# Optimization experiments

Hardware: AMD Instinct MI355X
Metric: run time of the kernel (lower is better)

The kernel has to match this reference:

```python
import jax, jax.numpy as jnp
import numpy as np

KERNEL = 8


def setup_inputs() -> dict:
    key = jax.random.key(0)
    ks = jax.random.split(key, 9)
    N, Cin, L = 16, 128, 2048
    Cout = 256
    x = jax.random.normal(ks[0], (N, Cin, L), dtype=jnp.float32)
    conv_w = jax.random.normal(ks[1], (Cout, Cin, KERNEL), dtype=jnp.float32) * (1.0 / np.sqrt(Cin * KERNEL))
    conv_b = jax.random.normal(ks[2], (Cout,), dtype=jnp.float32) * 0.01
    wq = jax.random.normal(ks[3], (Cout, Cout), dtype=jnp.float32) * (1.0 / np.sqrt(Cout))
    bq = jax.random.normal(ks[4], (Cout,), dtype=jnp.float32) * 0.01
    wk = jax.random.normal(ks[5], (Cout, Cout), dtype=jnp.float32) * (1.0 / np.sqrt(Cout))
    bk = jax.random.normal(ks[6], (Cout,), dtype=jnp.float32) * 0.01
    wv = jax.random.normal(ks[7], (Cout, Cout), dtype=jnp.float32) * (1.0 / np.sqrt(Cout))
    bv = jax.random.normal(ks[8], (Cout,), dtype=jnp.float32) * 0.01
    return {"x": x, "conv_w": conv_w, "conv_b": conv_b,
            "wq": wq, "bq": bq, "wk": wk, "bk": bk, "wv": wv, "bv": bv}


def reference(x, conv_w, conv_b, wq, bq, wk, bk, wv, bv):
    # Conv1d, valid padding: [N, Cin, L] -> [N, Cout, S], S = L - KERNEL + 1
    h = jax.lax.conv_general_dilated(
        x, conv_w, window_strides=(1,), padding='VALID',
        dimension_numbers=('NCH', 'OIH', 'NCH'))
    h = jax.nn.relu(h + conv_b[None, :, None])
    N, C, S = h.shape
    h = jnp.transpose(h, (0, 2, 1))  # [N, S, C]
    # Linear layers (torch convention: y = x @ W^T + b)
    q = jnp.einsum('nsc,dc->nsd', h, wq) + bq
    k = jnp.einsum('nsc,dc->nsd', h, wk) + bk
    v = jnp.einsum('nsc,dc->nsd', h, wv) + bv
    # sigmoid (non-normalized) attention over full SxS scores
    scores = jnp.einsum('nsd,ntd->nst', q, k) / jnp.sqrt(jnp.asarray(C, h.dtype))
    attn = jax.nn.sigmoid(scores)  # [N, S, S]
    out = jnp.einsum('nst,ntd->nsd', attn, v)
    return jnp.transpose(out, (0, 2, 1))  # [N, C, S]
```

## Files before the change

kernel.cpp:

```cpp
#include <hip/hip_runtime.h>

typedef short short8 __attribute__((ext_vector_type(8)));
typedef float f32x4 __attribute__((ext_vector_type(4)));
typedef float f32x16 __attribute__((ext_vector_type(16)));
typedef unsigned short u16x4 __attribute__((ext_vector_type(4)));

constexpr int NB = 16, CIN = 128, LIN = 2048, CO = 256;
constexpr int SL = 2041;
constexpr int MP = 32768;
constexpr int XTS = 136;


constexpr size_t XT_OFF = 0;
constexpr size_t XT_SZ  = (size_t)NB*LIN*XTS*2 + 65536;
constexpr size_t CW_OFF = XT_OFF + XT_SZ;
constexpr size_t CW_SZ  = (size_t)CO*CIN*8*2;
constexpr size_t WQ_OFF = CW_OFF + CW_SZ;
constexpr size_t WB_SZ  = (size_t)CO*CO*2;
constexpr size_t WK_OFF = WQ_OFF + WB_SZ;
constexpr size_t WV_OFF = WK_OFF + WB_SZ;
constexpr size_t H_OFF  = WV_OFF + WB_SZ;
constexpr size_t HB_SZ  = (size_t)MP*CO*2;
constexpr size_t Q_OFF  = H_OFF + HB_SZ;
constexpr size_t K_OFF  = Q_OFF + HB_SZ;
constexpr size_t VT_OFF = K_OFF + HB_SZ;

__device__ inline unsigned short f2bf(float f) {
  union { float f; unsigned int u; } v; v.f = f;
  unsigned int r = v.u + 0x7fffu + ((v.u >> 16) & 1u);
  return (unsigned short)(r >> 16);
}

__device__ inline void sync_lds() {
  __asm__ volatile("" ::: "memory");
  __builtin_amdgcn_s_waitcnt(0xc07f);
  __builtin_amdgcn_s_barrier();
  __asm__ volatile("" ::: "memory");
}
__device__ inline void barrier_only() {
  __asm__ volatile("" ::: "memory");
  __builtin_amdgcn_s_barrier();
  __asm__ volatile("" ::: "memory");
}

#if defined(__has_builtin)
#if __has_builtin(__builtin_amdgcn_global_load_lds)
#define HAVE_GLDS 1
#endif
#endif

__device__ inline void gld16(const unsigned short* g, void* l) {
#ifdef HAVE_GLDS
  __builtin_amdgcn_global_load_lds(
      (const __attribute__((address_space(1))) void*)g,
      (__attribute__((address_space(3))) void*)l, 16, 0, 0);
#else
  *(short8*)l = *(const short8*)g;
#endif
}

__global__ __launch_bounds__(256) void prep_kernel(
    const float* __restrict__ x, unsigned short* __restrict__ xt,
    const float* __restrict__ cw_in, unsigned short* __restrict__ cw_out,
    const float* __restrict__ wq, const float* __restrict__ wk, const float* __restrict__ wv,
    unsigned short* __restrict__ wqb, unsigned short* __restrict__ wkb,
    unsigned short* __restrict__ wvb) {
  __shared__ float tile[32][33];
  const int b = blockIdx.x;
  const int tid = threadIdx.x;
  if (b < 4096) {
    const int tx = tid & 31, ty = tid >> 5;
    const int s0 = (b & 63) * 32, c0 = ((b >> 6) & 3) * 32, n = b >> 8;
    #pragma unroll
    for (int r = 0; r < 4; ++r)
      tile[ty * 4 + r][tx] = x[((size_t)(n * CIN + c0 + ty * 4 + r)) * LIN + s0 + tx];
    __syncthreads();
    #pragma unroll
    for (int r = 0; r < 4; ++r)
      xt[((size_t)(n * LIN + s0 + ty * 4 + r)) * XTS + c0 + tx] = f2bf(tile[tx][ty * 4 + r]);
  } else if (b < 4096 + 1024) {
    int idx = (b - 4096) * 256 + tid;
    int co = idx >> 10, r = idx & 1023, kp = r >> 7, ci = r & 127;
    cw_out[idx] = f2bf(cw_in[co * 1024 + ci * 8 + kp]);
  } else {
    int lb2 = b - (4096 + 1024);
    int z = lb2 >> 6, lb = lb2 & 63;
    const float* src = (z == 0) ? wq : (z == 1) ? wk : wv;
    unsigned short* dst = (z == 0) ? wqb : (z == 1) ? wkb : wvb;
    int i = (lb * 256 + tid) * 4;
    float4 v = *(const float4*)(src + i);
    u16x4 r;
    r.x = f2bf(v.x); r.y = f2bf(v.y); r.z = f2bf(v.z); r.w = f2bf(v.w);
    *(u16x4*)(dst + i) = r;
  }
}

__global__ __launch_bounds__(256) void conv_gemm(
    const unsigned short* __restrict__ xt,
    const unsigned short* __restrict__ wb,
    const float* __restrict__ bias,
    unsigned short* __restrict__ h)
{
  __shared__ unsigned short sX[18432];
  __shared__ unsigned short sB[2][4096];
  const int tid = threadIdx.x;
  const int w = tid >> 6, lane = tid & 63, quad = lane >> 4, l16 = lane & 15;
  const int n  = blockIdx.y;
  const int s0 = blockIdx.x * 128;
  const int d0 = blockIdx.z * 128;

  {
    const unsigned short* xbase = xt + ((size_t)n * LIN + s0) * XTS;
    #pragma unroll
    for (int i = 0; i < 9; ++i) {
      int u = i * 256 + tid;
      gld16(xbase + u * 8, ((char*)sX) + u * 16);
    }
  }

  const int brow0 = tid >> 2, bkgs = tid & 3;
  short8 breg[2];
  #pragma unroll
  for (int i2 = 0; i2 < 2; ++i2) {
    int row = i2 * 64 + brow0;
    int kg = bkgs ^ ((row >> 1) & 3);
    breg[i2] = *(const short8*)(wb + (size_t)(d0 + row) * 1024 + kg * 8);
  }
  #pragma unroll
  for (int i2 = 0; i2 < 2; ++i2)
    *(short8*)(&sB[0][(i2 * 256 + tid) * 8]) = breg[i2];
  __syncthreads();

  f32x4 acc[2][8];
  #pragma unroll
  for (int i = 0; i < 2; ++i)
    #pragma unroll
    for (int j = 0; j < 8; ++j) acc[i][j] = (f32x4){0.f, 0.f, 0.f, 0.f};

  for (int kc = 0; kc < 32; ++kc) {
    const int kcn = (kc < 31) ? kc + 1 : kc;
    const int kpn = kcn >> 2, ci0n = (kcn & 3) * 32;
    #pragma unroll
    for (int i2 = 0; i2 < 2; ++i2) {
      int row = i2 * 64 + brow0;
      int kg = bkgs ^ ((row >> 1) & 3);
      breg[i2] = *(const short8*)(wb + (size_t)(d0 + row) * 1024 + kpn * 128 + ci0n + kg * 8);
    }

    const int kp = kc >> 2, ci0 = (kc & 3) * 32;
    const unsigned short* sBc = sB[kc & 1];
    short8 bfr[8];
    #pragma unroll
    for (int j = 0; j < 8; ++j) {
      int r = j * 16 + l16;
      bfr[j] = *(const short8*)(sBc + r * 32 + (quad ^ ((r >> 1) & 3)) * 8);
    }
    #pragma unroll
    for (int i = 0; i < 2; ++i) {
      int srow = w * 32 + i * 16 + l16;
      short8 afr = *(const short8*)(sX + (srow + kp) * XTS + ci0 + quad * 8);
      #pragma unroll
      for (int j = 0; j < 8; ++j)
        acc[i][j] = __builtin_amdgcn_mfma_f32_16x16x32_bf16(afr, bfr[j], acc[i][j], 0, 0, 0);
    }

    #pragma unroll
    for (int i2 = 0; i2 < 2; ++i2)
      *(short8*)(&sB[(kc + 1) & 1][(i2 * 256 + tid) * 8]) = breg[i2];
    sync_lds();
  }

  #pragma unroll
  for (int i = 0; i < 2; ++i)
    #pragma unroll
    for (int j = 0; j < 8; ++j) {
      int col = d0 + j * 16 + l16;
      float bv = bias[col];
      #pragma unroll
      for (int jj = 0; jj < 4; ++jj) {
        int s = s0 + w * 32 + i * 16 + quad * 4 + jj;
        if (s < SL) {
          float val = fmaxf(acc[i][j][jj] + bv, 0.f);
          h[(size_t)(n * 2048 + s) * CO + col] = f2bf(val);
        }
      }
    }
}

__global__ __launch_bounds__(256) void lin_gemm(
    const unsigned short* __restrict__ A,
    const unsigned short* __restrict__ Bq, const unsigned short* __restrict__ Bk,
    const unsigned short* __restrict__ Bv,
    const float* __restrict__ biq, const float* __restrict__ bik,
    const float* __restrict__ biv,
    unsigned short* __restrict__ qb, unsigned short* __restrict__ kb,
    unsigned short* __restrict__ vtb)
{
  __shared__ unsigned short smem[16384];
  unsigned short* const sAb = smem;
  unsigned short* const sBb = smem + 8192;
  const int tid = threadIdx.x;
  const int w = tid >> 6, lane = tid & 63, quad = lane >> 4, l16 = lane & 15;
  const int m0 = blockIdx.x * 128, d0 = blockIdx.y * 128, z = blockIdx.z;
  const unsigned short* B = (z == 0) ? Bq : (z == 1) ? Bk : Bv;
  const float* bias        = (z == 0) ? biq : (z == 1) ? bik : biv;

  const int brow0 = tid >> 2, bkgs = tid & 3;
  short8 areg[2], breg[2];
  #pragma unroll
  for (int i2 = 0; i2 < 2; ++i2) {
    int row = i2 * 64 + brow0;
    int kg = bkgs ^ ((row >> 1) & 3);
    areg[i2] = *(const short8*)(A + (size_t)(m0 + row) * CO + kg * 8);
    breg[i2] = *(const short8*)(B + (size_t)(d0 + row) * CO + kg * 8);
  }
  #pragma unroll
  for (int i2 = 0; i2 < 2; ++i2) {
    *(short8*)(sAb + (i2 * 256 + tid) * 8) = areg[i2];
    *(short8*)(sBb + (i2 * 256 + tid) * 8) = breg[i2];
  }
  sync_lds();

  f32x4 acc[2][8];
  #pragma unroll
  for (int i = 0; i < 2; ++i)
    #pragma unroll
    for (int j = 0; j < 8; ++j) acc[i][j] = (f32x4){0.f, 0.f, 0.f, 0.f};

  for (int kc = 0; kc < 8; ++kc) {
    const int kcn = (kc < 7) ? kc + 1 : kc;
    #pragma unroll
    for (int i2 = 0; i2 < 2; ++i2) {
      int row = i2 * 64 + brow0;
      int kg = bkgs ^ ((row >> 1) & 3);
      areg[i2] = *(const short8*)(A + (size_t)(m0 + row) * CO + kcn * 32 + kg * 8);
      breg[i2] = *(const short8*)(B + (size_t)(d0 + row) * CO + kcn * 32 + kg * 8);
    }

    const unsigned short* sAc = sAb + (kc & 1) * 4096;
    const unsigned short* sBc = sBb + (kc & 1) * 4096;
    short8 afr[2], bfr[8];
    #pragma unroll
    for (int i = 0; i < 2; ++i) {
      int r = w * 32 + i * 16 + l16;
      afr[i] = *(const short8*)(sAc + r * 32 + (quad ^ ((r >> 1) & 3)) * 8);
    }
    #pragma unroll
    for (int j = 0; j < 8; ++j) {
      int r = j * 16 + l16;
      bfr[j] = *(const short8*)(sBc + r * 32 + (quad ^ ((r >> 1) & 3)) * 8);
    }
    #pragma unroll
    for (int i = 0; i < 2; ++i)
      #pragma unroll
      for (int j = 0; j < 8; ++j)
        acc[i][j] = __builtin_amdgcn_mfma_f32_16x16x32_bf16(afr[i], bfr[j], acc[i][j], 0, 0, 0);

    #pragma unroll
    for (int i2 = 0; i2 < 2; ++i2) {
      *(short8*)(sAb + ((kc + 1) & 1) * 4096 + (i2 * 256 + tid) * 8) = areg[i2];
      *(short8*)(sBb + ((kc + 1) & 1) * 4096 + (i2 * 256 + tid) * 8) = breg[i2];
    }
    sync_lds();
  }

  if (z < 2) {
    #pragma unroll
    for (int i = 0; i < 2; ++i)
      #pragma unroll
      for (int j = 0; j < 8; ++j) {
        int col = d0 + j * 16 + l16;
        float bv = bias[col];
        #pragma unroll
        for (int jj = 0; jj < 4; ++jj) {
          int m = m0 + w * 32 + i * 16 + quad * 4 + jj;
          float val = acc[i][j][jj] + bv;
          ((z == 0) ? qb : kb)[(size_t)m * CO + col] = f2bf(val);
        }
      }
  } else {
    #pragma unroll
    for (int i = 0; i < 2; ++i)
      #pragma unroll
      for (int j = 0; j < 8; ++j) {
        int c = j * 16 + l16;
        float bv = bias[d0 + c];
        int mb = w * 32 + i * 16 + quad * 4;
        u16x4 pk;
        #pragma unroll
        for (int jj = 0; jj < 4; ++jj) pk[jj] = f2bf(acc[i][j][jj] + bv);
        *(u16x4*)(smem + c * 128 + (mb ^ ((c & 7) << 3))) = pk;
      }
    sync_lds();
    const int c = tid >> 1, mh = (tid & 1) * 64;
    const int nn = m0 >> 11;
    const int sbase = (m0 & 2047) + mh;
    unsigned short* vrow = vtb + (size_t)(d0 + c) * MP + nn * 2048;
    #pragma unroll
    for (int b = 0; b < 8; ++b) {
      int ss = sbase + b * 8;
      short8 val = *(const short8*)(smem + c * 128 + ((mh + b * 8) ^ ((c & 7) << 3)));
      if (ss + 7 >= SL) {
        #pragma unroll
        for (int e = 0; e < 8; ++e)
          if (ss + e >= SL) val[e] = 0;
      }
      *(short8*)(vrow + ss) = val;
    }
  }
}

__global__ __launch_bounds__(512, 2) void attn_kernel(
    const unsigned short* __restrict__ qb,
    const unsigned short* __restrict__ kb,
    const unsigned short* __restrict__ vtb,
    float* __restrict__ out)
{
  __shared__ unsigned short sK[2][16384];
  __shared__ unsigned short sV[2][16384];
  __shared__ unsigned short sP[8192];
  const int tid = threadIdx.x;
  const int w = tid >> 6, lane = tid & 63;
  const int half = lane >> 5, l32 = lane & 31;
  const int bidx = blockIdx.x;
  const int n = (bidx & 7) + ((bidx >> 7) << 3);
  const int s0 = ((bidx >> 3) & 15) * 128;
  const int sr = w & 3, tr = w >> 2;

  const unsigned short* kbN = kb + (size_t)(n * 2048) * CO;
  const unsigned short* vbN = vtb + (size_t)n * 2048;

#define STAGE_TILE(buf, tk)                                                      \
  {                                                                              \
    _Pragma("unroll")                                                            \
    for (int i = 0; i < 4; ++i) {                                                \
      int u = i * 512 + tid;                                                     \
      int t = u >> 5, sl = u & 31;                                               \
      gld16(kbN + (size_t)((tk) + t) * CO + ((sl ^ (t & 31)) << 3),              \
            ((char*)sK[buf]) + u * 16);                                          \
    }                                                                            \
    _Pragma("unroll")                                                            \
    for (int i = 0; i < 4; ++i) {                                                \
      int u = i * 512 + tid;                                                     \
      int d = u >> 3, sl = u & 7;                                                \
      gld16(vbN + (size_t)d * MP + (tk) + ((sl ^ (d & 7)) << 3),                 \
            ((char*)sV[buf]) + u * 16);                                          \
    }                                                                            \
  }

  STAGE_TILE(0, 0)

  short8 qf[16];
  {
    const unsigned short* qp = qb + (size_t)(n * 2048 + s0 + sr * 32 + l32) * CO + half * 8;
    #pragma unroll
    for (int kk = 0; kk < 16; ++kk) qf[kk] = *(const short8*)(qp + kk * 16);
  }

  __builtin_amdgcn_s_waitcnt(0x0F70);
  barrier_only();

  f32x16 o[4];
  #pragma unroll
  for (int di = 0; di < 4; ++di)
    #pragma unroll
    for (int r = 0; r < 16; ++r) o[di][r] = 0.f;

  for (int it = 0; it < 32; ++it) {
    const int cur = it & 1;
    if (it < 31) {
      STAGE_TILE(cur ^ 1, (it + 1) * 64)
      __builtin_amdgcn_s_waitcnt(0x0F78);
    } else {
      __builtin_amdgcn_s_waitcnt(0x0F70);
    }
    barrier_only();

    const unsigned short* sKc = sK[cur];
    const int tl = tr * 32 + l32;
    f32x16 sacc;
    #pragma unroll
    for (int r = 0; r < 16; ++r) sacc[r] = 0.f;
    #pragma unroll
    for (int kk = 0; kk < 16; ++kk) {
      short8 kf = *(const short8*)(sKc + tl * 256 + (((kk * 2 + half) ^ (tl & 31)) << 3));
      sacc = __builtin_amdgcn_mfma_f32_32x32x16_bf16(kf, qf[kk], sacc, 0, 0, 0);
    }

    const int t0 = it * 64;
    #pragma unroll
    for (int q2 = 0; q2 < 4; ++q2) {
      u16x4 pk;
      #pragma unroll
      for (int e = 0; e < 4; ++e) {
        int tg = t0 + tr * 32 + 8 * q2 + 4 * half + e;
        float p = __builtin_amdgcn_rcpf(1.f + __expf(-sacc[q2 * 4 + e] * 0.0625f));
        pk[e] = (tg < SL) ? f2bf(p) : (unsigned short)0;
      }
      *(u16x4*)(sP + ((tr * 4 + q2) * 128 + sr * 32 + l32) * 8 + 4 * half) = pk;
    }
    sync_lds();

    const unsigned short* sVc = sV[cur];
    #pragma unroll
    for (int kt = 0; kt < 4; ++kt) {
      int g = kt * 2 + half;
      short8 pa = *(const short8*)(sP + ((g << 7) + sr * 32 + l32) * 8);
      #pragma unroll
      for (int di = 0; di < 4; ++di) {
        int d = tr * 128 + di * 32 + l32;
        short8 vf = *(const short8*)(sVc + d * 64 + ((g ^ (d & 7)) << 3));
        o[di] = __builtin_amdgcn_mfma_f32_32x32x16_bf16(vf, pa, o[di], 0, 0, 0);
      }
    }
    sync_lds();
  }

  const int s = s0 + sr * 32 + l32;
  if (s < SL) {
    float* op = out + (size_t)n * CO * SL + s;
    #pragma unroll
    for (int di = 0; di < 4; ++di)
      #pragma unroll
      for (int r = 0; r < 16; ++r) {
        int d = tr * 128 + di * 32 + (r & 3) + 8 * (r >> 2) + 4 * half;
        __builtin_nontemporal_store(o[di][r], op + (size_t)d * SL);
      }
  }
#undef STAGE_TILE
}

extern "C" void kernel_launch(void* const* d_in, const int* in_sizes, int n_in,
                              void* d_out, int out_size, void* d_ws, size_t ws_size,
                              hipStream_t stream) {
  const float* x      = (const float*)d_in[0];
  const float* conv_w = (const float*)d_in[1];
  const float* conv_b = (const float*)d_in[2];
  const float* wq     = (const float*)d_in[3];
  const float* bq     = (const float*)d_in[4];
  const float* wk     = (const float*)d_in[5];
  const float* bk     = (const float*)d_in[6];
  const float* wv     = (const float*)d_in[7];
  const float* bv     = (const float*)d_in[8];

  char* ws = (char*)d_ws;
  unsigned short* xt  = (unsigned short*)(ws + XT_OFF);
  unsigned short* cw  = (unsigned short*)(ws + CW_OFF);
  unsigned short* wqb = (unsigned short*)(ws + WQ_OFF);
  unsigned short* wkb = (unsigned short*)(ws + WK_OFF);
  unsigned short* wvb = (unsigned short*)(ws + WV_OFF);
  unsigned short* hb  = (unsigned short*)(ws + H_OFF);
  unsigned short* qb  = (unsigned short*)(ws + Q_OFF);
  unsigned short* kb  = (unsigned short*)(ws + K_OFF);
  unsigned short* vtb = (unsigned short*)(ws + VT_OFF);

  hipLaunchKernelGGL(prep_kernel, dim3(4096 + 1024 + 192), dim3(256), 0, stream,
                     x, xt, conv_w, cw, wq, wk, wv, wqb, wkb, wvb);
  hipLaunchKernelGGL(conv_gemm, dim3(16, 16, 2), dim3(256), 0, stream, xt, cw, conv_b, hb);
  hipLaunchKernelGGL(lin_gemm,  dim3(256, 2, 3), dim3(256), 0, stream,
                     hb, wqb, wkb, wvb, bq, bk, bv, qb, kb, vtb);
  hipLaunchKernelGGL(attn_kernel, dim3(256), dim3(512), 0, stream,
                     qb, kb, vtb, (float*)d_out);
}
```

Before: 233.5 us.

## Fuse conv GEMM with QKV projections, keeping h tile in LDS

Measured after the change: 232.1 us, median of 3. Within noise of the previous version (-0.6%).

```diff
diff --git a/kernel.cpp b/kernel.cpp
--- a/kernel.cpp
+++ b/kernel.cpp
@@ -9,6 +9,7 @@
 constexpr int SL = 2041;
 constexpr int MP = 32768;
 constexpr int XTS = 136;
+constexpr int QSTR = 2048 * CO + 256;
 
 
 constexpr size_t XT_OFF = 0;
@@ -19,11 +20,10 @@
 constexpr size_t WB_SZ  = (size_t)CO*CO*2;
 constexpr size_t WK_OFF = WQ_OFF + WB_SZ;
 constexpr size_t WV_OFF = WK_OFF + WB_SZ;
-constexpr size_t H_OFF  = WV_OFF + WB_SZ;
-constexpr size_t HB_SZ  = (size_t)MP*CO*2;
-constexpr size_t Q_OFF  = H_OFF + HB_SZ;
-constexpr size_t K_OFF  = Q_OFF + HB_SZ;
-constexpr size_t VT_OFF = K_OFF + HB_SZ;
+constexpr size_t Q_OFF  = WV_OFF + WB_SZ;
+constexpr size_t QK_SZ  = (size_t)NB*QSTR*2 + 256;
+constexpr size_t K_OFF  = Q_OFF + QK_SZ;
+constexpr size_t VT_OFF = K_OFF + QK_SZ;
 
 __device__ inline unsigned short f2bf(float f) {
   union { float f; unsigned int u; } v; v.f = f;
@@ -95,100 +95,10 @@
   }
 }
 
-__global__ __launch_bounds__(256) void conv_gemm(
+__global__ __launch_bounds__(512, 2) void conv_qkv(
     const unsigned short* __restrict__ xt,
     const unsigned short* __restrict__ wb,
-    const float* __restrict__ bias,
-    unsigned short* __restrict__ h)
-{
-  __shared__ unsigned short sX[18432];
-  __shared__ unsigned short sB[2][4096];
-  const int tid = threadIdx.x;
-  const int w = tid >> 6, lane = tid & 63, quad = lane >> 4, l16 = lane & 15;
-  const int n  = blockIdx.y;
-  const int s0 = blockIdx.x * 128;
-  const int d0 = blockIdx.z * 128;
-
-  {
-    const unsigned short* xbase = xt + ((size_t)n * LIN + s0) * XTS;
-    #pragma unroll
-    for (int i = 0; i < 9; ++i) {
-      int u = i * 256 + tid;
-      gld16(xbase + u * 8, ((char*)sX) + u * 16);
-    }
-  }
-
-  const int brow0 = tid >> 2, bkgs = tid & 3;
-  short8 breg[2];
-  #pragma unroll
-  for (int i2 = 0; i2 < 2; ++i2) {
-    int row = i2 * 64 + brow0;
-    int kg = bkgs ^ ((row >> 1) & 3);
-    breg[i2] = *(const short8*)(wb + (size_t)(d0 + row) * 1024 + kg * 8);
-  }
-  #pragma unroll
-  for (int i2 = 0; i2 < 2; ++i2)
-    *(short8*)(&sB[0][(i2 * 256 + tid) * 8]) = breg[i2];
-  __syncthreads();
-
-  f32x4 acc[2][8];
-  #pragma unroll
-  for (int i = 0; i < 2; ++i)
-    #pragma unroll
-    for (int j = 0; j < 8; ++j) acc[i][j] = (f32x4){0.f, 0.f, 0.f, 0.f};
-
-  for (int kc = 0; kc < 32; ++kc) {
-    const int kcn = (kc < 31) ? kc + 1 : kc;
-    const int kpn = kcn >> 2, ci0n = (kcn & 3) * 32;
-    #pragma unroll
-    for (int i2 = 0; i2 < 2; ++i2) {
-      int row = i2 * 64 + brow0;
-      int kg = bkgs ^ ((row >> 1) & 3);
-      breg[i2] = *(const short8*)(wb + (size_t)(d0 + row) * 1024 + kpn * 128 + ci0n + kg * 8);
-    }
-
-    const int kp = kc >> 2, ci0 = (kc & 3) * 32;
-    const unsigned short* sBc = sB[kc & 1];
-    short8 bfr[8];
-    #pragma unroll
-    for (int j = 0; j < 8; ++j) {
-      int r = j * 16 + l16;
-      bfr[j] = *(const short8*)(sBc + r * 32 + (quad ^ ((r >> 1) & 3)) * 8);
-    }
-    #pragma unroll
-    for (int i = 0; i < 2; ++i) {
-      int srow = w * 32 + i * 16 + l16;
-      short8 afr = *(const short8*)(sX + (srow + kp) * XTS + ci0 + quad * 8);
-      #pragma unroll
-      for (int j = 0; j < 8; ++j)
-        acc[i][j] = __builtin_amdgcn_mfma_f32_16x16x32_bf16(afr, bfr[j], acc[i][j], 0, 0, 0);
-    }
-
-    #pragma unroll
-    for (int i2 = 0; i2 < 2; ++i2)
-      *(short8*)(&sB[(kc + 1) & 1][(i2 * 256 + tid) * 8]) = breg[i2];
-    sync_lds();
-  }
-
-  #pragma unroll
-  for (int i = 0; i < 2; ++i)
-    #pragma unroll
-    for (int j = 0; j < 8; ++j) {
-      int col = d0 + j * 16 + l16;
-      float bv = bias[col];
-      #pragma unroll
-      for (int jj = 0; jj < 4; ++jj) {
-        int s = s0 + w * 32 + i * 16 + quad * 4 + jj;
-        if (s < SL) {
-          float val = fmaxf(acc[i][j][jj] + bv, 0.f);
-          h[(size_t)(n * 2048 + s) * CO + col] = f2bf(val);
-        }
-      }
-    }
-}
-
-__global__ __launch_bounds__(256) void lin_gemm(
-    const unsigned short* __restrict__ A,
+    const float* __restrict__ cbias,
     const unsigned short* __restrict__ Bq, const unsigned short* __restrict__ Bk,
     const unsigned short* __restrict__ Bv,
     const float* __restrict__ biq, const float* __restrict__ bik,
@@ -196,30 +106,35 @@
     unsigned short* __restrict__ qb, unsigned short* __restrict__ kb,
     unsigned short* __restrict__ vtb)
 {
-  __shared__ unsigned short smem[16384];
-  unsigned short* const sAb = smem;
-  unsigned short* const sBb = smem + 8192;
+  __shared__ unsigned short hL[32768];
+  __shared__ unsigned short sX[18432];
+  __shared__ unsigned short sB[2][8192];
   const int tid = threadIdx.x;
   const int w = tid >> 6, lane = tid & 63, quad = lane >> 4, l16 = lane & 15;
-  const int m0 = blockIdx.x * 128, d0 = blockIdx.y * 128, z = blockIdx.z;
-  const unsigned short* B = (z == 0) ? Bq : (z == 1) ? Bk : Bv;
-  const float* bias        = (z == 0) ? biq : (z == 1) ? bik : biv;
+  const int sg = w >> 1, dh = w & 1;
+  const int n = blockIdx.y, s0 = blockIdx.x * 128;
+
+  {
+    const unsigned short* xbase = xt + ((size_t)n * LIN + s0) * XTS;
+    #pragma unroll
+    for (int i = 0; i < 5; ++i) {
+      int u = i * 512 + tid;
+      if (u < 2304) gld16(xbase + u * 8, ((char*)sX) + u * 16);
+    }
+  }
 
   const int brow0 = tid >> 2, bkgs = tid & 3;
-  short8 areg[2], breg[2];
+  short8 breg[2];
   #pragma unroll
   for (int i2 = 0; i2 < 2; ++i2) {
-    int row = i2 * 64 + brow0;
+    int row = i2 * 128 + brow0;
     int kg = bkgs ^ ((row >> 1) & 3);
-    areg[i2] = *(const short8*)(A + (size_t)(m0 + row) * CO + kg * 8);
-    breg[i2] = *(const short8*)(B + (size_t)(d0 + row) * CO + kg * 8);
+    breg[i2] = *(const short8*)(wb + (size_t)row * 1024 + kg * 8);
   }
   #pragma unroll
-  for (int i2 = 0; i2 < 2; ++i2) {
-    *(short8*)(sAb + (i2 * 256 + tid) * 8) = areg[i2];
-    *(short8*)(sBb + (i2 * 256 + tid) * 8) = breg[i2];
-  }
-  sync_lds();
+  for (int i2 = 0; i2 < 2; ++i2)
+    *(short8*)(&sB[0][(i2 * 512 + tid) * 8]) = breg[i2];
+  __syncthreads();
 
   f32x4 acc[2][8];
   #pragma unroll
@@ -227,85 +142,150 @@
     #pragma unroll
     for (int j = 0; j < 8; ++j) acc[i][j] = (f32x4){0.f, 0.f, 0.f, 0.f};
 
-  for (int kc = 0; kc < 8; ++kc) {
-    const int kcn = (kc < 7) ? kc + 1 : kc;
+  for (int kc = 0; kc < 32; ++kc) {
+    const int kcn = (kc < 31) ? kc + 1 : kc;
+    const int kpn = kcn >> 2, ci0n = (kcn & 3) * 32;
     #pragma unroll
     for (int i2 = 0; i2 < 2; ++i2) {
-      int row = i2 * 64 + brow0;
+      int row = i2 * 128 + brow0;
       int kg = bkgs ^ ((row >> 1) & 3);
-      areg[i2] = *(const short8*)(A + (size_t)(m0 + row) * CO + kcn * 32 + kg * 8);
-      breg[i2] = *(const short8*)(B + (size_t)(d0 + row) * CO + kcn * 32 + kg * 8);
-    }
-
-    const unsigned short* sAc = sAb + (kc & 1) * 4096;
-    const unsigned short* sBc = sBb + (kc & 1) * 4096;
-    short8 afr[2], bfr[8];
+      breg[i2] = *(const short8*)(wb + (size_t)row * 1024 + kpn * 128 + ci0n + kg * 8);
+    }
+
+    const int kp = kc >> 2, ci0 = (kc & 3) * 32;
+    const unsigned short* sBc = sB[kc & 1];
+    short8 bfr[8];
+    #pragma unroll
+    for (int j = 0; j < 8; ++j) {
+      int r = dh * 128 + j * 16 + l16;
+      bfr[j] = *(const short8*)(sBc + r * 32 + (quad ^ ((r >> 1) & 3)) * 8);
+    }
     #pragma unroll
     for (int i = 0; i < 2; ++i) {
-      int r = w * 32 + i * 16 + l16;
-      afr[i] = *(const short8*)(sAc + r * 32 + (quad ^ ((r >> 1) & 3)) * 8);
-    }
+      int srow = sg * 32 + i * 16 + l16;
+      short8 afr = *(const short8*)(sX + (srow + kp) * XTS + ci0 + quad * 8);
+      #pragma unroll
+      for (int j = 0; j < 8; ++j)
+        acc[i][j] = __builtin_amdgcn_mfma_f32_16x16x32_bf16(afr, bfr[j], acc[i][j], 0, 0, 0);
+    }
+
+    #pragma unroll
+    for (int i2 = 0; i2 < 2; ++i2)
+      *(short8*)(&sB[(kc + 1) & 1][(i2 * 512 + tid) * 8]) = breg[i2];
+    sync_lds();
+  }
+
+  #pragma unroll
+  for (int i = 0; i < 2; ++i)
     #pragma unroll
     for (int j = 0; j < 8; ++j) {
-      int r = j * 16 + l16;
-      bfr[j] = *(const short8*)(sBc + r * 32 + (quad ^ ((r >> 1) & 3)) * 8);
-    }
+      int c = dh * 128 + j * 16 + l16;
+      float bv = cbias[c];
+      int cc = (c >> 5) * 32 + (c & 7);
+      int g = (c >> 3) & 3;
+      #pragma unroll
+      for (int jj = 0; jj < 4; ++jj) {
+        int r = sg * 32 + i * 16 + quad * 4 + jj;
+        hL[r * 256 + cc + ((g ^ ((r >> 1) & 3)) << 3)] =
+            f2bf(fmaxf(acc[i][j][jj] + bv, 0.f));
+      }
+    }
+
+  for (int z = 0; z < 3; ++z) {
+    const unsigned short* B = (z == 0) ? Bq : (z == 1) ? Bk : Bv;
+    const float* bias        = (z == 0) ? biq : (z == 1) ? bik : biv;
+
+    #pragma unroll
+    for (int i2 = 0; i2 < 2; ++i2) {
+      int row = i2 * 128 + brow0;
+      int kg = bkgs ^ ((row >> 1) & 3);
+      breg[i2] = *(const short8*)(B + (size_t)row * CO + kg * 8);
+    }
+    #pragma unroll
+    for (int i2 = 0; i2 < 2; ++i2)
+      *(short8*)(&sB[0][(i2 * 512 + tid) * 8]) = breg[i2];
+    sync_lds();
+
     #pragma unroll
     for (int i = 0; i < 2; ++i)
       #pragma unroll
-      for (int j = 0; j < 8; ++j)
-        acc[i][j] = __builtin_amdgcn_mfma_f32_16x16x32_bf16(afr[i], bfr[j], acc[i][j], 0, 0, 0);
-
-    #pragma unroll
-    for (int i2 = 0; i2 < 2; ++i2) {
-      *(short8*)(sAb + ((kc + 1) & 1) * 4096 + (i2 * 256 + tid) * 8) = areg[i2];
-      *(short8*)(sBb + ((kc + 1) & 1) * 4096 + (i2 * 256 + tid) * 8) = breg[i2];
-    }
-    sync_lds();
-  }
-
-  if (z < 2) {
-    #pragma unroll
-    for (int i = 0; i < 2; ++i)
+      for (int j = 0; j < 8; ++j) acc[i][j] = (f32x4){0.f, 0.f, 0.f, 0.f};
+
+    for (int kc = 0; kc < 8; ++kc) {
+      const int kcn = (kc < 7) ? kc + 1 : kc;
+      #pragma unroll
+      for (int i2 = 0; i2 < 2; ++i2) {
+        int row = i2 * 128 + brow0;
+        int kg = bkgs ^ ((row >> 1) & 3);
+        breg[i2] = *(const short8*)(B + (size_t)row * CO + kcn * 32 + kg * 8);
+      }
+
+      const unsigned short* sBc = sB[kc & 1];
+      short8 afr[2], bfr[8];
+      #pragma unroll
+      for (int i = 0; i < 2; ++i) {
+        int r = sg * 32 + i * 16 + l16;
+        afr[i] = *(const short8*)(hL + r * 256 + kc * 32 + (quad ^ ((r >> 1) & 3)) * 8);
+      }
       #pragma unroll
       for (int j = 0; j < 8; ++j) {
-        int col = d0 + j * 16 + l16;
-        float bv = bias[col];
+        int r = dh * 128 + j * 16 + l16;
+        bfr[j] = *(const short8*)(sBc + r * 32 + (quad ^ ((r >> 1) & 3)) * 8);
+      }
+      #pragma unroll
+      for (int i = 0; i < 2; ++i)
         #pragma unroll
-        for (int jj = 0; jj < 4; ++jj) {
-          int m = m0 + w * 32 + i * 16 + quad * 4 + jj;
-          float val = acc[i][j][jj] + bv;
-          ((z == 0) ? qb : kb)[(size_t)m * CO + col] = f2bf(val);
+        for (int j = 0; j < 8; ++j)
+          acc[i][j] = __builtin_amdgcn_mfma_f32_16x16x32_bf16(afr[i], bfr[j], acc[i][j], 0, 0, 0);
+
+      #pragma unroll
+      for (int i2 = 0; i2 < 2; ++i2)
+        *(short8*)(&sB[(kc + 1) & 1][(i2 * 512 + tid) * 8]) = breg[i2];
+      sync_lds();
+    }
+
+    if (z < 2) {
+      unsigned short* base = ((z == 0) ? qb : kb) + (size_t)n * QSTR + (size_t)s0 * CO;
+      #pragma unroll
+      for (int i = 0; i < 2; ++i)
+        #pragma unroll
+        for (int j = 0; j < 8; ++j) {
+          int c = dh * 128 + j * 16 + l16;
+          float bv = bias[c];
+          #pragma unroll
+          for (int jj = 0; jj < 4; ++jj) {
+            int r = sg * 32 + i * 16 + quad * 4 + jj;
+            base[(size_t)r * CO + c] = f2bf(acc[i][j][jj] + bv);
+          }
         }
-      }
-  } else {
-    #pragma unroll
-    for (int i = 0; i < 2; ++i)
-      #pragma unroll
-      for (int j = 0; j < 8; ++j) {
-        int c = j * 16 + l16;
-        float bv = bias[d0 + c];
-        int mb = w * 32 + i * 16 + quad * 4;
-        u16x4 pk;
+    } else {
+      #pragma unroll
+      for (int i = 0; i < 2; ++i)
         #pragma unroll
-        for (int jj = 0; jj < 4; ++jj) pk[jj] = f2bf(acc[i][j][jj] + bv);
-        *(u16x4*)(smem + c * 128 + (mb ^ ((c & 7) << 3))) = pk;
-      }
-    sync_lds();
-    const int c = tid >> 1, mh = (tid & 1) * 64;
-    const int nn = m0 >> 11;
-    const int sbase = (m0 & 2047) + mh;
-    unsigned short* vrow = vtb + (size_t)(d0 + c) * MP + nn * 2048;
-    #pragma unroll
-    for (int b = 0; b < 8; ++b) {
-      int ss = sbase + b * 8;
-      short8 val = *(const short8*)(smem + c * 128 + ((mh + b * 8) ^ ((c & 7) << 3)));
-      if (ss + 7 >= SL) {
-        #pragma unroll
-        for (int e = 0; e < 8; ++e)
-          if (ss + e >= SL) val[e] = 0;
-      }
-      *(short8*)(vrow + ss) = val;
+        for (int j = 0; j < 8; ++j) {
+          int c = dh * 128 + j * 16 + l16;
+          float bv = bias[c];
+          int mb = sg * 32 + i * 16 + quad * 4;
+          u16x4 pk;
+          #pragma unroll
+          for (int jj = 0; jj < 4; ++jj) pk[jj] = f2bf(acc[i][j][jj] + bv);
+          *(u16x4*)(hL + c * 128 + (mb ^ ((c & 7) << 3))) = pk;
+        }
+      sync_lds();
+      const int c = tid >> 1, mh = (tid & 1) * 64;
+      unsigned short* vrow = vtb + (size_t)c * MP + n * 2048 + s0;
+      #pragma unroll
+      for (int b = 0; b < 8; ++b) {
+        int ml = mh + b * 8;
+        int ss = s0 + ml;
+        short8 val = *(const short8*)(hL + c * 128 + (ml ^ ((c & 7) << 3)));
+        if (ss + 7 >= SL) {
+          #pragma unroll
+          for (int e = 0; e < 8; ++e)
+            if (ss + e >= SL) val[e] = 0;
+        }
+        *(short8*)(vrow + ml) = val;
+      }
     }
   }
 }
@@ -327,7 +307,7 @@
   const int s0 = ((bidx >> 3) & 15) * 128;
   const int sr = w & 3, tr = w >> 2;
 
-  const unsigned short* kbN = kb + (size_t)(n * 2048) * CO;
+  const unsigned short* kbN = kb + (size_t)n * QSTR;
   const unsigned short* vbN = vtb + (size_t)n * 2048;
 
 #define STAGE_TILE(buf, tk)                                                      \
@@ -352,7 +332,8 @@
 
   short8 qf[16];
   {
-    const unsigned short* qp = qb + (size_t)(n * 2048 + s0 + sr * 32 + l32) * CO + half * 8;
+    const unsigned short* qp = qb + (size_t)n * QSTR
+                             + (size_t)(s0 + sr * 32 + l32) * CO + half * 8;
     #pragma unroll
     for (int kk = 0; kk < 16; ++kk) qf[kk] = *(const short8*)(qp + kk * 16);
   }
@@ -449,16 +430,14 @@
   unsigned short* wqb = (unsigned short*)(ws + WQ_OFF);
   unsigned short* wkb = (unsigned short*)(ws + WK_OFF);
   unsigned short* wvb = (unsigned short*)(ws + WV_OFF);
-  unsigned short* hb  = (unsigned short*)(ws + H_OFF);
   unsigned short* qb  = (unsigned short*)(ws + Q_OFF);
   unsigned short* kb  = (unsigned short*)(ws + K_OFF);
   unsigned short* vtb = (unsigned short*)(ws + VT_OFF);
 
   hipLaunchKernelGGL(prep_kernel, dim3(4096 + 1024 + 192), dim3(256), 0, stream,
                      x, xt, conv_w, cw, wq, wk, wv, wqb, wkb, wvb);
-  hipLaunchKernelGGL(conv_gemm, dim3(16, 16, 2), dim3(256), 0, stream, xt, cw, conv_b, hb);
-  hipLaunchKernelGGL(lin_gemm,  dim3(256, 2, 3), dim3(256), 0, stream,
-                     hb, wqb, wkb, wvb, bq, bk, bv, qb, kb, vtb);
+  hipLaunchKernelGGL(conv_qkv, dim3(16, 16), dim3(512), 0, stream,
+                     xt, cw, conv_b, wqb, wkb, wvb, bq, bk, bv, qb, kb, vtb);
   hipLaunchKernelGGL(attn_kernel, dim3(256), dim3(512), 0, stream,
                      qb, kb, vtb, (float*)d_out);
 }
```
